# Kernel tuning notes

Measured on AMD Instinct MI355X. Metric: run time of the kernel, lower is better.

## Reference

```python
import jax, jax.numpy as jnp
import numpy as np

N_LEVELS = 1024
K = 8  # number of spike timesteps; d/T have length K+1 (index 0 unused)
X_SHAPE = (64, 512, 1024)


def setup_inputs() -> dict:
    key = jax.random.key(0)
    kx, kh0, kh, kd, kT = jax.random.split(key, 5)
    x = jax.random.normal(kx, X_SHAPE, dtype=jnp.float32) * 2.0
    # h: [N_LEVELS, K+1]; column 0 is the sorted search grid (required by searchsorted)
    h0 = jnp.sort(jax.random.uniform(kh0, (N_LEVELS,), minval=-4.0, maxval=4.0))
    h = jax.random.normal(kh, (N_LEVELS, K + 1), dtype=jnp.float32)
    h = h.at[:, 0].set(h0)
    d = jax.random.uniform(kd, (K + 1,), minval=0.05, maxval=1.0)
    T = jax.random.uniform(kT, (K + 1,), minval=-1.0, maxval=1.0)
    b = jnp.float32(0.1)
    return {"x": x, "h": h, "d": d, "T": T, "b": b}


def reference(x, h, d, T, b):
    sp = x.shape
    xf = x.reshape(-1)
    grid = h[:, 0]  # sorted lookup grid
    n = grid.shape[0]
    idx = jnp.clip(jnp.searchsorted(grid, xf), 1, n - 1)
    left = grid[idx - 1]
    right = grid[idx]
    take_left = jnp.abs(xf - left) < jnp.abs(xf - right)
    nearest = jnp.where(take_left, left, right)          # quantized input
    nidx = jnp.where(take_left, idx - 1, idx)            # per-element row into h
    kmax = d.shape[0] - 1
    v = nearest
    out = jnp.zeros_like(xf)
    # loop over the small fixed number of thresholds (data dims fully vectorized)
    for t in range(1, kmax + 1):
        z = (v - T[t] >= 0).astype(xf.dtype)
        out = out + z * d[t]
        if t != kmax:
            v = h[nidx, t + 1]  # irregular per-element gather
    out = out - b
    return out.reshape(sp)
```

## Files before the change

kernel.cpp:

```cpp
#include <hip/hip_runtime.h>
#include <math.h>

#define NL  1024
#define KP1 9
#define NB  4096

#define WS_PAIR 4
#define WS_BKT  (WS_PAIR + 2*(NL+8))

__device__ __forceinline__ unsigned oi(float f) {
    unsigned u = __float_as_uint(f);
    return (u & 0x80000000u) ? ~u : (u | 0x80000000u);
}
__device__ __forceinline__ float unoi(unsigned k) {
    return __uint_as_float((k & 0x80000000u) ? (k & 0x7fffffffu) : ~k);
}

__device__ __forceinline__ int bidx(float x, float lo0, float inv) {
    float t = (x - lo0) * inv;
    int j = (int)t;
    j = j < 0 ? 0 : j;
    j = j > (NB - 1) ? (NB - 1) : j;
    return j;
}

__global__ __launch_bounds__(1024) void build_kernel(
    const float* __restrict__ h, const float* __restrict__ d,
    const float* __restrict__ T, const float* __restrict__ bp,
    float* __restrict__ ws)
{
    __shared__ float s_g[NL];
    __shared__ float s_B[NL];
    __shared__ int   s_jb[NL];
    __shared__ float s_lo0, s_inv;

    const int tid = threadIdx.x;
    float g = h[tid * KP1];
    s_g[tid] = g;

    float outv;
    {
        float v = g, o = 0.0f, b = bp[0];
#pragma unroll
        for (int t = 1; t <= 8; ++t) {
            float z = ((v - T[t]) >= 0.0f) ? 1.0f : 0.0f;
            o = o + z * d[t];
            if (t != 8) v = h[tid * KP1 + (t + 1)];
        }
        outv = o - b;
    }
    __syncthreads();

    if (tid < NL - 1) {
        float l = s_g[tid], r = s_g[tid + 1];
        unsigned a = oi(l), b2 = oi(r);
        while (a < b2) {
            unsigned m = a + ((b2 - a) >> 1);
            float xm = unoi(m);
            float dl = fabsf(xm - l), dr = fabsf(xm - r);
            if (!(dl < dr)) b2 = m; else a = m + 1;
        }
        s_B[tid] = unoi(a);
    } else {
        s_B[tid] = INFINITY;
    }
    __syncthreads();

    if (tid == 0) {
        float lo0 = s_B[0];
        float inv = (float)NB / (s_B[NL - 2] - lo0);
        s_lo0 = lo0; s_inv = inv;
        ws[0] = lo0; ws[1] = inv;
    }
    __syncthreads();

    float lo0 = s_lo0, inv = s_inv;
    s_jb[tid] = (tid < NL - 1) ? bidx(s_B[tid], lo0, inv) : 0x7fffffff;

    ws[WS_PAIR + 2 * tid]     = s_B[tid];
    ws[WS_PAIR + 2 * tid + 1] = outv;
    if (tid < 8) {
        ws[WS_PAIR + 2 * (NL + tid)]     = INFINITY;
        ws[WS_PAIR + 2 * (NL + tid) + 1] = 0.0f;
    }
    __syncthreads();

    unsigned short* bucket = (unsigned short*)(ws + WS_BKT);
    for (int j = tid; j < NB; j += 1024) {
        int lo = 0;
#pragma unroll
        for (int s = 512; s >= 1; s >>= 1)
            if (s_jb[lo + s - 1] < j) lo += s;
        bucket[j] = (unsigned short)lo;
    }
}

typedef float vf4 __attribute__((ext_vector_type(4)));

__device__ __forceinline__ float4 proc4(float4 v,
                                        const float2* __restrict__ pp,
                                        const unsigned short* __restrict__ sbk,
                                        float lo0, float inv)
{
    int n0 = sbk[bidx(v.x, lo0, inv)];
    int n1 = sbk[bidx(v.y, lo0, inv)];
    int n2 = sbk[bidx(v.z, lo0, inv)];
    int n3 = sbk[bidx(v.w, lo0, inv)];
    float2 a0 = pp[n0], b0 = pp[n0 + 1];
    float2 a1 = pp[n1], b1 = pp[n1 + 1];
    float2 a2 = pp[n2], b2 = pp[n2 + 1];
    float2 a3 = pp[n3], b3 = pp[n3 + 1];
    float r0 = (a0.x > v.x) ? a0.y : b0.y;
    float r1 = (a1.x > v.x) ? a1.y : b1.y;
    r1 = (a1.x > v.y) ? a1.y : b1.y;
    float r2 = (a2.x > v.z) ? a2.y : b2.y;
    float r3 = (a3.x > v.w) ? a3.y : b3.y;
    bool f0 = (b0.x <= v.x), f1 = (b1.x <= v.y);
    bool f2 = (b2.x <= v.z), f3 = (b3.x <= v.w);
    if (__builtin_expect(f0 | f1 | f2 | f3, 0)) {
        if (f0) { int m = n0 + 2; float2 p = pp[m];
                  while (p.x <= v.x) { ++m; p = pp[m]; } r0 = p.y; }
        if (f1) { int m = n1 + 2; float2 p = pp[m];
                  while (p.x <= v.y) { ++m; p = pp[m]; } r1 = p.y; }
        if (f2) { int m = n2 + 2; float2 p = pp[m];
                  while (p.x <= v.z) { ++m; p = pp[m]; } r2 = p.y; }
        if (f3) { int m = n3 + 2; float2 p = pp[m];
                  while (p.x <= v.w) { ++m; p = pp[m]; } r3 = p.y; }
    }
    return make_float4(r0, r1, r2, r3);
}

__global__ __launch_bounds__(256) void ps_act_kernel(
    const float* __restrict__ x,
    const float* __restrict__ ws,
    float* __restrict__ out,
    int n4)
{
    __shared__ __align__(16) float          spair[2 * (NL + 8)];
    __shared__ __align__(16) unsigned short sbk[NB];

    const int tid = threadIdx.x;
    {
        const float4* wp4 = (const float4*)(ws + WS_PAIR);
        float4* sp4 = (float4*)spair;
        for (int i = tid; i < 2 * (NL + 8) / 4; i += 256) sp4[i] = wp4[i];
        const uint4* wb4 = (const uint4*)(ws + WS_BKT);
        uint4* sb4 = (uint4*)sbk;
        for (int i = tid; i < NB * 2 / 16; i += 256) sb4[i] = wb4[i];
    }
    const float lo0 = ws[0];
    const float inv = ws[1];
    __syncthreads();

    const float4* __restrict__ x4 = (const float4*)x;
    float4* __restrict__ o4 = (float4*)out;
    const float2* pp = (const float2*)spair;
    const int stride = gridDim.x * blockDim.x;

    for (int i4 = blockIdx.x * blockDim.x + tid; i4 < n4; i4 += 2 * stride) {
        const int j4 = i4 + stride;
        float4 c0 = x4[i4];
        float4 c1 = make_float4(0.f, 0.f, 0.f, 0.f);
        if (j4 < n4) c1 = x4[j4];

        float4 r0 = proc4(c0, pp, sbk, lo0, inv);
        vf4 o0 = {r0.x, r0.y, r0.z, r0.w};
        __builtin_nontemporal_store(o0, (vf4*)&o4[i4]);

        if (j4 < n4) {
            float4 r1 = proc4(c1, pp, sbk, lo0, inv);
            vf4 o1 = {r1.x, r1.y, r1.z, r1.w};
            __builtin_nontemporal_store(o1, (vf4*)&o4[j4]);
        }
    }
}

extern "C" void kernel_launch(void* const* d_in, const int* in_sizes, int n_in,
                              void* d_out, int out_size, void* d_ws, size_t ws_size,
                              hipStream_t stream) {
    const float* x = (const float*)d_in[0];
    const float* h = (const float*)d_in[1];
    const float* d = (const float*)d_in[2];
    const float* T = (const float*)d_in[3];
    const float* b = (const float*)d_in[4];
    float* out = (float*)d_out;
    float* ws  = (float*)d_ws;

    int n  = in_sizes[0];
    int n4 = n / 4;

    build_kernel<<<1, 1024, 0, stream>>>(h, d, T, b, ws);
    ps_act_kernel<<<4096, 256, 0, stream>>>(x, ws, out, n4);
}
```

Before: 250.6 us.

## Stage input through LDS with async global_load_lds multi-buffer pipeline

Replaces the grid-stride register loads with a fully unrolled 8-step loop when the size matches exactly 8 strides. Input tiles are prefetched straight into a 4-slot LDS buffer with global_load_lds, and manual vmcnt waits overlap the loads with the lookup work. The bucket table is also halved to shrink the shared-memory footprint. The extra 16 KB of LDS per block may reduce occupancy, and the hand-tuned vmcnt counts rely on store/load counter behavior.

```diff
diff --git a/kernel.cpp b/kernel.cpp
--- a/kernel.cpp
+++ b/kernel.cpp
@@ -3,7 +3,7 @@
 
 #define NL  1024
 #define KP1 9
-#define NB  4096
+#define NB  2048
 
 #define WS_PAIR 4
 #define WS_BKT  (WS_PAIR + 2*(NL+8))
@@ -96,6 +96,8 @@
 }
 
 typedef float vf4 __attribute__((ext_vector_type(4)));
+
+#define WAIT_VMCNT(n) asm volatile("s_waitcnt vmcnt(" #n ")" ::: "memory")
 
 __device__ __forceinline__ float4 proc4(float4 v,
                                         const float2* __restrict__ pp,
@@ -111,8 +113,7 @@
     float2 a2 = pp[n2], b2 = pp[n2 + 1];
     float2 a3 = pp[n3], b3 = pp[n3 + 1];
     float r0 = (a0.x > v.x) ? a0.y : b0.y;
-    float r1 = (a1.x > v.x) ? a1.y : b1.y;
-    r1 = (a1.x > v.y) ? a1.y : b1.y;
+    float r1 = (a1.x > v.y) ? a1.y : b1.y;
     float r2 = (a2.x > v.z) ? a2.y : b2.y;
     float r3 = (a3.x > v.w) ? a3.y : b3.y;
     bool f0 = (b0.x <= v.x), f1 = (b1.x <= v.y);
@@ -138,6 +139,7 @@
 {
     __shared__ __align__(16) float          spair[2 * (NL + 8)];
     __shared__ __align__(16) unsigned short sbk[NB];
+    __shared__ __align__(16) float          xbuf[4 * 1024];
 
     const int tid = threadIdx.x;
     {
@@ -156,21 +158,56 @@
     float4* __restrict__ o4 = (float4*)out;
     const float2* pp = (const float2*)spair;
     const int stride = gridDim.x * blockDim.x;
-
-    for (int i4 = blockIdx.x * blockDim.x + tid; i4 < n4; i4 += 2 * stride) {
-        const int j4 = i4 + stride;
-        float4 c0 = x4[i4];
-        float4 c1 = make_float4(0.f, 0.f, 0.f, 0.f);
-        if (j4 < n4) c1 = x4[j4];
-
-        float4 r0 = proc4(c0, pp, sbk, lo0, inv);
-        vf4 o0 = {r0.x, r0.y, r0.z, r0.w};
-        __builtin_nontemporal_store(o0, (vf4*)&o4[i4]);
-
-        if (j4 < n4) {
-            float4 r1 = proc4(c1, pp, sbk, lo0, inv);
-            vf4 o1 = {r1.x, r1.y, r1.z, r1.w};
-            __builtin_nontemporal_store(o1, (vf4*)&o4[j4]);
+    const int gbase  = blockIdx.x * blockDim.x + tid;
+    const int wslot  = (tid >> 6) << 8;
+
+    if (n4 == 8 * stride) {
+#pragma unroll
+        for (int t = 0; t < 4; ++t)
+            __builtin_amdgcn_global_load_lds(
+                (const float*)(x4 + ((long)t * stride + gbase)),
+                &xbuf[t * 1024 + wslot], 16, 0, 0);
+        asm volatile("" ::: "memory");
+
+#define STEP(t, WAITMACRO, PREFETCH)                                        \
+        {                                                                   \
+            WAITMACRO;                                                      \
+            float4 c = *(const float4*)&xbuf[((t) & 3) * 1024 + (tid << 2)];\
+            float4 r = proc4(c, pp, sbk, lo0, inv);                         \
+            vf4 oo = {r.x, r.y, r.z, r.w};                                  \
+            __builtin_nontemporal_store(                                    \
+                oo, (vf4*)&o4[(long)(t) * stride + gbase]);                 \
+            if (PREFETCH)                                                   \
+                __builtin_amdgcn_global_load_lds(                           \
+                    (const float*)(x4 + ((long)((t)+4) * stride + gbase)),  \
+                    &xbuf[((t) & 3) * 1024 + wslot], 16, 0, 0);             \
+            asm volatile("" ::: "memory");                                  \
+        }
+        STEP(0, WAIT_VMCNT(3), 1)
+        STEP(1, WAIT_VMCNT(4), 1)
+        STEP(2, WAIT_VMCNT(5), 1)
+        STEP(3, WAIT_VMCNT(6), 1)
+        STEP(4, WAIT_VMCNT(6), 0)
+        STEP(5, WAIT_VMCNT(5), 0)
+        STEP(6, WAIT_VMCNT(4), 0)
+        STEP(7, WAIT_VMCNT(3), 0)
+#undef STEP
+    } else {
+        for (int i4 = gbase; i4 < n4; i4 += 2 * stride) {
+            const int j4 = i4 + stride;
+            float4 c0 = x4[i4];
+            float4 c1 = make_float4(0.f, 0.f, 0.f, 0.f);
+            if (j4 < n4) c1 = x4[j4];
+
+            float4 r0 = proc4(c0, pp, sbk, lo0, inv);
+            vf4 o0 = {r0.x, r0.y, r0.z, r0.w};
+            __builtin_nontemporal_store(o0, (vf4*)&o4[i4]);
+
+            if (j4 < n4) {
+                float4 r1 = proc4(c1, pp, sbk, lo0, inv);
+                vf4 o1 = {r1.x, r1.y, r1.z, r1.w};
+                __builtin_nontemporal_store(o1, (vf4*)&o4[j4]);
+            }
         }
     }
 }
```

Result: no change. 254.3 us (+1.5%).
